# Kernel optimization log

Hardware: AMD Instinct MI355X
Metric: run time of the kernel (lower is better)

The kernel has to match this reference:

```python
import jax, jax.numpy as jnp
import numpy as np

N, C_IN, H, W = 32, 16, 256, 256
C_OUT, K = 64, 3

def setup_inputs() -> dict:
    key = jax.random.key(0)
    kx, kw, kb = jax.random.split(key, 3)
    x = jax.random.normal(kx, (N, C_IN, H, W), dtype=jnp.float32)
    # PyTorch Conv2d default init: U(-b, b), b = 1/sqrt(fan_in)
    bound = 1.0 / np.sqrt(C_IN * K * K)
    conv_weight = jax.random.uniform(kw, (C_OUT, C_IN, K, K), minval=-bound, maxval=bound, dtype=jnp.float32)
    conv_bias = jax.random.uniform(kb, (C_OUT,), minval=-bound, maxval=bound, dtype=jnp.float32)
    return {"x": x, "conv_weight": conv_weight, "conv_bias": conv_bias}

def reference(x, conv_weight, conv_bias):
    # conv2d, stride=1, padding=0 (VALID), NCHW / OIHW
    y = jax.lax.conv_general_dilated(
        x, conv_weight,
        window_strides=(1, 1), padding="VALID",
        dimension_numbers=("NCHW", "OIHW", "NCHW"))
    y = y + conv_bias[None, :, None, None]
    # min over output channels (keepdim -> 1 channel), then double tanh
    y = jnp.min(y, axis=1, keepdims=True)  # [N,1,OH,OW]
    return jnp.tanh(jnp.tanh(y))
```

## Files before the change

kernel.cpp:

```cpp
#include <hip/hip_runtime.h>

typedef __bf16 bf16x8 __attribute__((ext_vector_type(8)));
typedef unsigned short us8 __attribute__((ext_vector_type(8)));
typedef unsigned short us2 __attribute__((ext_vector_type(2)));
typedef float f32x16 __attribute__((ext_vector_type(16)));

#define N_IMG 32
#define CI 16
#define HH 256
#define WW 256
#define CO 64
#define OHH 254
#define OWW 254

#define XS_W 258
#define SC 16
#define NSTRIP 24
#define WP_SHORTS (CO * 160)
#define WS_NEEDED ((size_t)WP_SHORTS * 2)

__device__ __forceinline__ unsigned short f2bf(float f) {
  union { float f; unsigned u; } v; v.f = f;
  return (unsigned short)((v.u + 0x7FFFu + ((v.u >> 16) & 1u)) >> 16);
}

#if defined(__has_builtin)
#if __has_builtin(__builtin_amdgcn_cvt_pk_bf16_f32)
#define HAVE_CVT_PK 1
#endif
#endif

__device__ __forceinline__ us2 cvt2(float a, float b) {
#ifdef HAVE_CVT_PK
  typedef __bf16 bf16x2 __attribute__((ext_vector_type(2)));
  bf16x2 r = __builtin_amdgcn_cvt_pk_bf16_f32(a, b);
  return __builtin_bit_cast(us2, r);
#else
  us2 r; r[0] = f2bf(a); r[1] = f2bf(b); return r;
#endif
}

__device__ __forceinline__ float fast_tanh(float x) {
  float cx = fminf(fmaxf(x, -15.f), 15.f);
  float e = __expf(2.f * cx);
  return (e - 1.f) / (e + 1.f);
}

__global__ void prep_w(const float* __restrict__ wg, const float* __restrict__ bg,
                       unsigned short* __restrict__ wp) {
  int idx = blockIdx.x * 256 + threadIdx.x;
  if (idx >= WP_SHORTS) return;
  int oc = idx / 160;
  int k = idx - oc * 160;
  int tap = k >> 4, ci = k & 15;
  float v;
  if (tap < 9)      v = wg[oc * 144 + ci * 9 + tap];
  else if (ci == 0) v = bg[oc];
  else              v = 0.f;
  wp[idx] = f2bf(v);
}

__global__ __launch_bounds__(256, 3)
void conv_fused(const float* __restrict__ xg, const unsigned short* __restrict__ wp,
                float* __restrict__ out) {
  __shared__ __align__(16) unsigned short xs[4 * XS_W * SC];
  const int t = threadIdx.x;
  const int n = blockIdx.x / NSTRIP;
  const int s = blockIdx.x - n * NSTRIP;
  const int oh0 = s * 10 + (s < 14 ? s : 14);
  const int nrows = (s < 14) ? 11 : 10;
  const int oh1 = oh0 + nrows;

  const float* srcT = xg + (size_t)n * (CI * HH * WW) + t;

  {
    float v[3][16];
#pragma unroll
    for (int r = 0; r < 3; ++r)
#pragma unroll
      for (int j = 0; j < 16; ++j)
        v[r][j] = srcT[((size_t)j * HH + (oh0 + r)) * WW];
#pragma unroll
    for (int r = 0; r < 3; ++r) {
      union { us8 v8[2]; us2 v2[8]; } pk;
#pragma unroll
      for (int j = 0; j < 8; ++j) pk.v2[j] = cvt2(v[r][2 * j], v[r][2 * j + 1]);
      const int slot = (oh0 + r) & 3;
      *(us8*)(xs + (slot * XS_W + t) * SC) = pk.v8[0];
      *(us8*)(xs + (slot * XS_W + t) * SC + 8) = pk.v8[1];
    }
  }
  if (t < 128) {
    const int slot = t >> 5, rem = t & 31;
    xs[(slot * XS_W + 256 + (rem >> 4)) * SC + (rem & 15)] = 0;
  }

  const int lane = t & 63, wave = t >> 6;
  const int lr = lane & 31, qh = lane >> 5;

  const unsigned short* wpl = wp + lr * 160 + qh * 8;
  bf16x8 afrag[2][10];
#pragma unroll
  for (int mt = 0; mt < 2; ++mt)
#pragma unroll
    for (int tap = 0; tap < 10; ++tap)
      afrag[mt][tap] =
          __builtin_bit_cast(bf16x8, *(const us8*)(wpl + mt * 32 * 160 + tap * 16));

  us8 onev = {};
  if (qh == 0) onev[0] = 0x3F80;
  const bf16x8 xone = __builtin_bit_cast(bf16x8, onev);

  const int pb = wave * 64;

  __syncthreads();

  for (int oh = oh0; oh < oh1; ++oh) {
    const bool do_stage = (oh + 1 < oh1);

    float v[16];
    if (do_stage) {
#pragma unroll
      for (int j = 0; j < 16; ++j)
        v[j] = srcT[((size_t)j * HH + (oh + 3)) * WW];
    }

    float vmin[2];
#pragma unroll
    for (int nt = 0; nt < 2; ++nt) {
      f32x16 acc0, acc1;
#pragma unroll
      for (int e = 0; e < 16; ++e) { acc0[e] = 0.f; acc1[e] = 0.f; }
#pragma unroll
      for (int tap = 0; tap < 9; ++tap) {
        const int kh = tap / 3, kw = tap - kh * 3;
        const int slot = (oh + kh) & 3;
        bf16x8 xf = __builtin_bit_cast(
            bf16x8,
            *(const us8*)(xs + (slot * XS_W + pb + nt * 32 + lr + kw) * SC + qh * 8));
        acc0 = __builtin_amdgcn_mfma_f32_32x32x16_bf16(afrag[0][tap], xf, acc0, 0, 0, 0);
        acc1 = __builtin_amdgcn_mfma_f32_32x32x16_bf16(afrag[1][tap], xf, acc1, 0, 0, 0);
      }
      acc0 = __builtin_amdgcn_mfma_f32_32x32x16_bf16(afrag[0][9], xone, acc0, 0, 0, 0);
      acc1 = __builtin_amdgcn_mfma_f32_32x32x16_bf16(afrag[1][9], xone, acc1, 0, 0, 0);

      float mv = acc0[0];
#pragma unroll
      for (int e = 1; e < 16; ++e) mv = fminf(mv, acc0[e]);
#pragma unroll
      for (int e = 0; e < 16; ++e) mv = fminf(mv, acc1[e]);
      mv = fminf(mv, __shfl_xor(mv, 32, 64));
      vmin[nt] = fast_tanh(fast_tanh(mv));
    }

    if (do_stage) {
      union { us8 v8[2]; us2 v2[8]; } pk;
#pragma unroll
      for (int j = 0; j < 8; ++j) pk.v2[j] = cvt2(v[2 * j], v[2 * j + 1]);
      const int slot = (oh + 3) & 3;
      *(us8*)(xs + (slot * XS_W + t) * SC) = pk.v8[0];
      *(us8*)(xs + (slot * XS_W + t) * SC + 8) = pk.v8[1];
    }

    const float res = (lane < 32) ? vmin[0] : vmin[1];
    const int ow = pb + lane;
    if (ow < OWW) out[((size_t)n * OHH + oh) * OWW + ow] = res;

    __syncthreads();
  }
}

#define XS_C 24
#define WS_K 168
__global__ __launch_bounds__(256, 2)
void conv_min_tanh(const float* __restrict__ xg, const float* __restrict__ wg,
                   const float* __restrict__ bg, float* __restrict__ out) {
  __shared__ __align__(16) unsigned short xs[3 * XS_W * XS_C];
  __shared__ __align__(16) unsigned short ws[CO * WS_K];
  const int t = threadIdx.x;
  const int n = blockIdx.x / OHH;
  const int oh = blockIdx.x % OHH;
#pragma unroll
  for (int i = 0; i < 36; ++i) {
    int f = i * 256 + t;
    int oc = f / 144;
    int r = f - oc * 144;
    int ci = r / 9;
    int tap = r - ci * 9;
    ws[oc * WS_K + tap * 16 + ci] = f2bf(wg[f]);
  }
  if (t < CO) ws[t * WS_K + 144] = f2bf(bg[t]);
  for (int i = t; i < CO * 15; i += 256) {
    int oc = i / 15;
    ws[oc * WS_K + 145 + (i - oc * 15)] = 0;
  }
  {
    const size_t base_n = (size_t)n * CI * HH * WW;
#pragma unroll
    for (int kh = 0; kh < 3; ++kh) {
#pragma unroll
      for (int half = 0; half < 2; ++half) {
        float v[8];
#pragma unroll
        for (int j = 0; j < 8; ++j) {
          int ci = half * 8 + j;
          v[j] = xg[base_n + ((size_t)ci * HH + (oh + kh)) * WW + t];
        }
        us8 pk;
#pragma unroll
        for (int j = 0; j < 8; ++j) pk[j] = f2bf(v[j]);
        *(us8*)(xs + (kh * XS_W + t) * XS_C + half * 8) = pk;
      }
    }
  }
  if (t < 96) {
    int kh = t >> 5;
    int rem = t & 31;
    int w = 256 + (rem >> 4);
    int ci = rem & 15;
    xs[(kh * XS_W + w) * XS_C + ci] = 0;
  }
  __syncthreads();
  const int lane = t & 63, wave = t >> 6;
  const int lr = lane & 31, qh = lane >> 5;
  bf16x8 afrag[2][10];
#pragma unroll
  for (int mt = 0; mt < 2; ++mt) {
    const unsigned short* wq = ws + (mt * 32 + lr) * WS_K + qh * 8;
#pragma unroll
    for (int tap = 0; tap < 10; ++tap)
      afrag[mt][tap] = __builtin_bit_cast(bf16x8, *(const us8*)(wq + tap * 16));
  }
  f32x16 acc[2][2];
#pragma unroll
  for (int a = 0; a < 2; ++a)
#pragma unroll
    for (int b = 0; b < 2; ++b)
#pragma unroll
      for (int e = 0; e < 16; ++e) acc[a][b][e] = 0.f;
  const unsigned short* xq = xs + (wave * 64 + lr) * XS_C + qh * 8;
#pragma unroll
  for (int tap = 0; tap < 9; ++tap) {
    const int kh = tap / 3, kw = tap - kh * 3;
#pragma unroll
    for (int nt = 0; nt < 2; ++nt) {
      bf16x8 xf = __builtin_bit_cast(
          bf16x8, *(const us8*)(xq + (kh * XS_W + nt * 32 + kw) * XS_C));
      acc[0][nt] = __builtin_amdgcn_mfma_f32_32x32x16_bf16(afrag[0][tap], xf,
                                                           acc[0][nt], 0, 0, 0);
      acc[1][nt] = __builtin_amdgcn_mfma_f32_32x32x16_bf16(afrag[1][tap], xf,
                                                           acc[1][nt], 0, 0, 0);
    }
  }
  {
    us8 one = {};
    if (qh == 0) one[0] = 0x3F80;
    bf16x8 xone = __builtin_bit_cast(bf16x8, one);
#pragma unroll
    for (int nt = 0; nt < 2; ++nt) {
      acc[0][nt] = __builtin_amdgcn_mfma_f32_32x32x16_bf16(afrag[0][9], xone,
                                                           acc[0][nt], 0, 0, 0);
      acc[1][nt] = __builtin_amdgcn_mfma_f32_32x32x16_bf16(afrag[1][9], xone,
                                                           acc[1][nt], 0, 0, 0);
    }
  }
  float vmin[2];
#pragma unroll
  for (int nt = 0; nt < 2; ++nt) {
    float v = acc[0][nt][0];
#pragma unroll
    for (int e = 1; e < 16; ++e) v = fminf(v, acc[0][nt][e]);
#pragma unroll
    for (int e = 0; e < 16; ++e) v = fminf(v, acc[1][nt][e]);
    v = fminf(v, __shfl_xor(v, 32, 64));
    vmin[nt] = fast_tanh(fast_tanh(v));
  }
  float res = (lane < 32) ? vmin[0] : vmin[1];
  int ow = wave * 64 + lane;
  if (ow < OWW) out[((size_t)n * OHH + oh) * OWW + ow] = res;
}

extern "C" void kernel_launch(void* const* d_in, const int* in_sizes, int n_in,
                              void* d_out, int out_size, void* d_ws, size_t ws_size,
                              hipStream_t stream) {
  const float* x = (const float*)d_in[0];
  const float* w = (const float*)d_in[1];
  const float* b = (const float*)d_in[2];
  float* out = (float*)d_out;
  if (ws_size >= WS_NEEDED) {
    unsigned short* wp = (unsigned short*)d_ws;
    prep_w<<<dim3((WP_SHORTS + 255) / 256), dim3(256), 0, stream>>>(w, b, wp);
    conv_fused<<<dim3(N_IMG * NSTRIP), dim3(256), 0, stream>>>(x, wp, out);
  } else {
    conv_min_tanh<<<dim3(N_IMG * OHH), dim3(256), 0, stream>>>(x, w, b, out);
  }
}
```

Before: 208.2 us.

## Fuse weight prep into conv kernel and double-buffer global row prefetch

```diff
diff --git a/kernel.cpp b/kernel.cpp
--- a/kernel.cpp
+++ b/kernel.cpp
@@ -14,10 +14,9 @@
 #define OWW 254
 
 #define XS_W 258
-#define SC 16
+#define SC 24
 #define NSTRIP 24
-#define WP_SHORTS (CO * 160)
-#define WS_NEEDED ((size_t)WP_SHORTS * 2)
+#define WS_K 168
 
 __device__ __forceinline__ unsigned short f2bf(float f) {
   union { float f; unsigned u; } v; v.f = f;
@@ -46,23 +45,9 @@
   return (e - 1.f) / (e + 1.f);
 }
 
-__global__ void prep_w(const float* __restrict__ wg, const float* __restrict__ bg,
-                       unsigned short* __restrict__ wp) {
-  int idx = blockIdx.x * 256 + threadIdx.x;
-  if (idx >= WP_SHORTS) return;
-  int oc = idx / 160;
-  int k = idx - oc * 160;
-  int tap = k >> 4, ci = k & 15;
-  float v;
-  if (tap < 9)      v = wg[oc * 144 + ci * 9 + tap];
-  else if (ci == 0) v = bg[oc];
-  else              v = 0.f;
-  wp[idx] = f2bf(v);
-}
-
 __global__ __launch_bounds__(256, 3)
-void conv_fused(const float* __restrict__ xg, const unsigned short* __restrict__ wp,
-                float* __restrict__ out) {
+void conv_fused(const float* __restrict__ xg, const float* __restrict__ wg,
+                const float* __restrict__ bg, float* __restrict__ out) {
   __shared__ __align__(16) unsigned short xs[4 * XS_W * SC];
   const int t = threadIdx.x;
   const int n = blockIdx.x / NSTRIP;
@@ -71,6 +56,43 @@
   const int nrows = (s < 14) ? 11 : 10;
   const int oh1 = oh0 + nrows;
 
+  const int lane = t & 63, wave = t >> 6;
+  const int lr = lane & 31, qh = lane >> 5;
+  const int pb = wave * 64;
+
+  {
+    unsigned short* wst = xs;
+#pragma unroll
+    for (int i = 0; i < 36; ++i) {
+      int f = i * 256 + t;
+      int oc = f / 144;
+      int r = f - oc * 144;
+      int ci = r / 9;
+      int tap = r - ci * 9;
+      wst[oc * WS_K + tap * 16 + ci] = f2bf(wg[f]);
+    }
+    if (t < CO) wst[t * WS_K + 144] = f2bf(bg[t]);
+    for (int i = t; i < CO * 15; i += 256) {
+      int oc = i / 15;
+      wst[oc * WS_K + 145 + (i - oc * 15)] = 0;
+    }
+  }
+  __syncthreads();
+
+  bf16x8 afrag[2][10];
+#pragma unroll
+  for (int mt = 0; mt < 2; ++mt) {
+    const unsigned short* wq = xs + (mt * 32 + lr) * WS_K + qh * 8;
+#pragma unroll
+    for (int tap = 0; tap < 10; ++tap)
+      afrag[mt][tap] = __builtin_bit_cast(bf16x8, *(const us8*)(wq + tap * 16));
+  }
+  __syncthreads();
+
+  us8 onev = {};
+  if (qh == 0) onev[0] = 0x3F80;
+  const bf16x8 xone = __builtin_bit_cast(bf16x8, onev);
+
   const float* srcT = xg + (size_t)n * (CI * HH * WW) + t;
 
   {
@@ -95,189 +117,79 @@
     xs[(slot * XS_W + 256 + (rem >> 4)) * SC + (rem & 15)] = 0;
   }
 
-  const int lane = t & 63, wave = t >> 6;
-  const int lr = lane & 31, qh = lane >> 5;
-
-  const unsigned short* wpl = wp + lr * 160 + qh * 8;
-  bf16x8 afrag[2][10];
-#pragma unroll
-  for (int mt = 0; mt < 2; ++mt)
-#pragma unroll
-    for (int tap = 0; tap < 10; ++tap)
-      afrag[mt][tap] =
-          __builtin_bit_cast(bf16x8, *(const us8*)(wpl + mt * 32 * 160 + tap * 16));
-
-  us8 onev = {};
-  if (qh == 0) onev[0] = 0x3F80;
-  const bf16x8 xone = __builtin_bit_cast(bf16x8, onev);
-
-  const int pb = wave * 64;
-
-  __syncthreads();
-
-  for (int oh = oh0; oh < oh1; ++oh) {
-    const bool do_stage = (oh + 1 < oh1);
-
-    float v[16];
-    if (do_stage) {
-#pragma unroll
-      for (int j = 0; j < 16; ++j)
-        v[j] = srcT[((size_t)j * HH + (oh + 3)) * WW];
-    }
-
-    float vmin[2];
-#pragma unroll
-    for (int nt = 0; nt < 2; ++nt) {
-      f32x16 acc0, acc1;
-#pragma unroll
-      for (int e = 0; e < 16; ++e) { acc0[e] = 0.f; acc1[e] = 0.f; }
-#pragma unroll
-      for (int tap = 0; tap < 9; ++tap) {
-        const int kh = tap / 3, kw = tap - kh * 3;
-        const int slot = (oh + kh) & 3;
-        bf16x8 xf = __builtin_bit_cast(
-            bf16x8,
-            *(const us8*)(xs + (slot * XS_W + pb + nt * 32 + lr + kw) * SC + qh * 8));
-        acc0 = __builtin_amdgcn_mfma_f32_32x32x16_bf16(afrag[0][tap], xf, acc0, 0, 0, 0);
-        acc1 = __builtin_amdgcn_mfma_f32_32x32x16_bf16(afrag[1][tap], xf, acc1, 0, 0, 0);
-      }
-      acc0 = __builtin_amdgcn_mfma_f32_32x32x16_bf16(afrag[0][9], xone, acc0, 0, 0, 0);
-      acc1 = __builtin_amdgcn_mfma_f32_32x32x16_bf16(afrag[1][9], xone, acc1, 0, 0, 0);
-
-      float mv = acc0[0];
-#pragma unroll
-      for (int e = 1; e < 16; ++e) mv = fminf(mv, acc0[e]);
-#pragma unroll
-      for (int e = 0; e < 16; ++e) mv = fminf(mv, acc1[e]);
-      mv = fminf(mv, __shfl_xor(mv, 32, 64));
-      vmin[nt] = fast_tanh(fast_tanh(mv));
-    }
-
-    if (do_stage) {
-      union { us8 v8[2]; us2 v2[8]; } pk;
-#pragma unroll
-      for (int j = 0; j < 8; ++j) pk.v2[j] = cvt2(v[2 * j], v[2 * j + 1]);
-      const int slot = (oh + 3) & 3;
-      *(us8*)(xs + (slot * XS_W + t) * SC) = pk.v8[0];
-      *(us8*)(xs + (slot * XS_W + t) * SC + 8) = pk.v8[1];
-    }
-
-    const float res = (lane < 32) ? vmin[0] : vmin[1];
-    const int ow = pb + lane;
-    if (ow < OWW) out[((size_t)n * OHH + oh) * OWW + ow] = res;
-
-    __syncthreads();
-  }
-}
-
-#define XS_C 24
-#define WS_K 168
-__global__ __launch_bounds__(256, 2)
-void conv_min_tanh(const float* __restrict__ xg, const float* __restrict__ wg,
-                   const float* __restrict__ bg, float* __restrict__ out) {
-  __shared__ __align__(16) unsigned short xs[3 * XS_W * XS_C];
-  __shared__ __align__(16) unsigned short ws[CO * WS_K];
-  const int t = threadIdx.x;
-  const int n = blockIdx.x / OHH;
-  const int oh = blockIdx.x % OHH;
-#pragma unroll
-  for (int i = 0; i < 36; ++i) {
-    int f = i * 256 + t;
-    int oc = f / 144;
-    int r = f - oc * 144;
-    int ci = r / 9;
-    int tap = r - ci * 9;
-    ws[oc * WS_K + tap * 16 + ci] = f2bf(wg[f]);
-  }
-  if (t < CO) ws[t * WS_K + 144] = f2bf(bg[t]);
-  for (int i = t; i < CO * 15; i += 256) {
-    int oc = i / 15;
-    ws[oc * WS_K + 145 + (i - oc * 15)] = 0;
-  }
-  {
-    const size_t base_n = (size_t)n * CI * HH * WW;
-#pragma unroll
-    for (int kh = 0; kh < 3; ++kh) {
-#pragma unroll
-      for (int half = 0; half < 2; ++half) {
-        float v[8];
-#pragma unroll
-        for (int j = 0; j < 8; ++j) {
-          int ci = half * 8 + j;
-          v[j] = xg[base_n + ((size_t)ci * HH + (oh + kh)) * WW + t];
-        }
-        us8 pk;
-#pragma unroll
-        for (int j = 0; j < 8; ++j) pk[j] = f2bf(v[j]);
-        *(us8*)(xs + (kh * XS_W + t) * XS_C + half * 8) = pk;
-      }
-    }
-  }
-  if (t < 96) {
-    int kh = t >> 5;
-    int rem = t & 31;
-    int w = 256 + (rem >> 4);
-    int ci = rem & 15;
-    xs[(kh * XS_W + w) * XS_C + ci] = 0;
-  }
-  __syncthreads();
-  const int lane = t & 63, wave = t >> 6;
-  const int lr = lane & 31, qh = lane >> 5;
-  bf16x8 afrag[2][10];
-#pragma unroll
-  for (int mt = 0; mt < 2; ++mt) {
-    const unsigned short* wq = ws + (mt * 32 + lr) * WS_K + qh * 8;
-#pragma unroll
-    for (int tap = 0; tap < 10; ++tap)
-      afrag[mt][tap] = __builtin_bit_cast(bf16x8, *(const us8*)(wq + tap * 16));
-  }
-  f32x16 acc[2][2];
-#pragma unroll
-  for (int a = 0; a < 2; ++a)
-#pragma unroll
-    for (int b = 0; b < 2; ++b)
-#pragma unroll
-      for (int e = 0; e < 16; ++e) acc[a][b][e] = 0.f;
-  const unsigned short* xq = xs + (wave * 64 + lr) * XS_C + qh * 8;
-#pragma unroll
-  for (int tap = 0; tap < 9; ++tap) {
-    const int kh = tap / 3, kw = tap - kh * 3;
-#pragma unroll
-    for (int nt = 0; nt < 2; ++nt) {
-      bf16x8 xf = __builtin_bit_cast(
-          bf16x8, *(const us8*)(xq + (kh * XS_W + nt * 32 + kw) * XS_C));
-      acc[0][nt] = __builtin_amdgcn_mfma_f32_32x32x16_bf16(afrag[0][tap], xf,
-                                                           acc[0][nt], 0, 0, 0);
-      acc[1][nt] = __builtin_amdgcn_mfma_f32_32x32x16_bf16(afrag[1][tap], xf,
-                                                           acc[1][nt], 0, 0, 0);
-    }
-  }
-  {
-    us8 one = {};
-    if (qh == 0) one[0] = 0x3F80;
-    bf16x8 xone = __builtin_bit_cast(bf16x8, one);
-#pragma unroll
-    for (int nt = 0; nt < 2; ++nt) {
-      acc[0][nt] = __builtin_amdgcn_mfma_f32_32x32x16_bf16(afrag[0][9], xone,
-                                                           acc[0][nt], 0, 0, 0);
-      acc[1][nt] = __builtin_amdgcn_mfma_f32_32x32x16_bf16(afrag[1][9], xone,
-                                                           acc[1][nt], 0, 0, 0);
-    }
-  }
-  float vmin[2];
-#pragma unroll
-  for (int nt = 0; nt < 2; ++nt) {
-    float v = acc[0][nt][0];
-#pragma unroll
-    for (int e = 1; e < 16; ++e) v = fminf(v, acc[0][nt][e]);
-#pragma unroll
-    for (int e = 0; e < 16; ++e) v = fminf(v, acc[1][nt][e]);
-    v = fminf(v, __shfl_xor(v, 32, 64));
-    vmin[nt] = fast_tanh(fast_tanh(v));
-  }
-  float res = (lane < 32) ? vmin[0] : vmin[1];
-  int ow = wave * 64 + lane;
-  if (ow < OWW) out[((size_t)n * OHH + oh) * OWW + ow] = res;
+  float vA[16], vB[16];
+#pragma unroll
+  for (int j = 0; j < 16; ++j)
+    vA[j] = srcT[((size_t)j * HH + (oh0 + 3)) * WW];
+
+  asm volatile("s_waitcnt lgkmcnt(0)" ::: "memory");
+  __builtin_amdgcn_s_barrier();
+  __builtin_amdgcn_sched_barrier(0);
+
+#define STEP(OH, CUR, NXT)                                                    \
+  {                                                                           \
+    const int oh_ = (OH);                                                     \
+    const bool do_stage = (oh_ + 1 < oh1);           \
+    const bool do_load = (oh_ + 2 < oh1);         \
+    if (do_load) {                                                            \
+      _Pragma("unroll")                                                       \
+      for (int j = 0; j < 16; ++j)                                            \
+        NXT[j] = srcT[((size_t)j * HH + (oh_ + 4)) * WW];                     \
+    }                                                                         \
+    __builtin_amdgcn_sched_barrier(0);        \
+    float vmin[2];                                                            \
+    _Pragma("unroll")                                                         \
+    for (int nt = 0; nt < 2; ++nt) {                                          \
+      float mv = 0.f;                                                         \
+      _Pragma("unroll")                                                       \
+      for (int mt = 0; mt < 2; ++mt) {                                        \
+        f32x16 acc;                                                           \
+        _Pragma("unroll")                                                     \
+        for (int e = 0; e < 16; ++e) acc[e] = 0.f;                            \
+        _Pragma("unroll")                                                     \
+        for (int tap = 0; tap < 9; ++tap) {                                   \
+          const int kh = tap / 3, kw = tap - kh * 3;                          \
+          const int slot = (oh_ + kh) & 3;                                    \
+          bf16x8 xf = __builtin_bit_cast(                                     \
+              bf16x8, *(const us8*)(xs + (slot * XS_W + pb + nt * 32 + lr +   \
+                                          kw) * SC + qh * 8));                \
+          acc = __builtin_amdgcn_mfma_f32_32x32x16_bf16(afrag[mt][tap], xf,   \
+                                                        acc, 0, 0, 0);        \
+        }                                                                     \
+        acc = __builtin_amdgcn_mfma_f32_32x32x16_bf16(afrag[mt][9], xone,     \
+                                                      acc, 0, 0, 0);          \
+        float m0 = acc[0];                                                    \
+        _Pragma("unroll")                                                     \
+        for (int e = 1; e < 16; ++e) m0 = fminf(m0, acc[e]);                  \
+        mv = (mt == 0) ? m0 : fminf(mv, m0);                                  \
+      }                                                                       \
+      mv = fminf(mv, __shfl_xor(mv, 32, 64));                                 \
+      vmin[nt] = fast_tanh(fast_tanh(mv));                                    \
+    }                                                                         \
+    if (do_stage) {        \
+      union { us8 v8[2]; us2 v2[8]; } pk;                                     \
+      _Pragma("unroll")                                                       \
+      for (int j = 0; j < 8; ++j) pk.v2[j] = cvt2(CUR[2 * j], CUR[2 * j + 1]);\
+      const int slot = (oh_ + 3) & 3;                                         \
+      *(us8*)(xs + (slot * XS_W + t) * SC) = pk.v8[0];                        \
+      *(us8*)(xs + (slot * XS_W + t) * SC + 8) = pk.v8[1];                    \
+    }                                                                         \
+    const float res = (lane < 32) ? vmin[0] : vmin[1];                        \
+    const int ow = pb + lane;                                                 \
+    if (ow < OWW) out[((size_t)n * OHH + oh_) * OWW + ow] = res;              \
+    asm volatile("s_waitcnt lgkmcnt(0)" ::: "memory");                        \
+    __builtin_amdgcn_s_barrier();                      \
+    __builtin_amdgcn_sched_barrier(0);                                        \
+  }
+
+  int oh = oh0;
+  for (;;) {
+    STEP(oh, vA, vB);
+    if (++oh >= oh1) break;
+    STEP(oh, vB, vA);
+    if (++oh >= oh1) break;
+  }
+#undef STEP
 }
 
 extern "C" void kernel_launch(void* const* d_in, const int* in_sizes, int n_in,
@@ -287,11 +199,6 @@
   const float* w = (const float*)d_in[1];
   const float* b = (const float*)d_in[2];
   float* out = (float*)d_out;
-  if (ws_size >= WS_NEEDED) {
-    unsigned short* wp = (unsigned short*)d_ws;
-    prep_w<<<dim3((WP_SHORTS + 255) / 256), dim3(256), 0, stream>>>(w, b, wp);
-    conv_fused<<<dim3(N_IMG * NSTRIP), dim3(256), 0, stream>>>(x, wp, out);
-  } else {
-    conv_min_tanh<<<dim3(N_IMG * OHH), dim3(256), 0, stream>>>(x, w, b, out);
-  }
-}
+  (void)d_ws; (void)ws_size;
+  conv_fused<<<dim3(N_IMG * NSTRIP), dim3(256), 0, stream>>>(x, w, b, out);
+}
```

New measurement: 325.0 us. 56.1% more time.
